# Kernel optimization log

Hardware: AMD Instinct MI355X
Metric: run time of the kernel (lower is better)

The kernel has to match this reference:

```python
import jax, jax.numpy as jnp
import numpy as np

N_SAMPLES = 64000
SAMPLE_RATE = 16000
DEPTH = 64              # bins per sinusoid in frequencies_softmax
HZ_MIN, HZ_MAX = 20.0, 8000.0


def exp_sigmoid(x, exponent=10.0, max_value=2.0, threshold=1e-7):
    # ddsp.core.exp_sigmoid
    return max_value * jax.nn.sigmoid(x) ** jnp.log(exponent) + threshold


def unit_to_hz(unit):
    # log-scale (midi) mapping of [0,1] -> [HZ_MIN, HZ_MAX]
    midi_min = 69.0 + 12.0 * np.log2(HZ_MIN / 440.0)
    midi_max = 69.0 + 12.0 * np.log2(HZ_MAX / 440.0)
    midi = midi_min + unit * (midi_max - midi_min)
    return 440.0 * 2.0 ** ((midi - 69.0) / 12.0)


def frequencies_softmax(logits):
    # ddsp.core.frequencies_softmax: softmax attention over DEPTH unit bins per sinusoid
    b, t, nd = logits.shape
    logits = logits.reshape(b, t, nd // DEPTH, DEPTH)
    probs = jax.nn.softmax(logits, axis=-1)
    bins = jnp.linspace(0.0, 1.0, DEPTH).astype(logits.dtype)
    f_unit = jnp.sum(probs * bins, axis=-1)          # [B, T, N]
    return unit_to_hz(f_unit)


def upsample_with_windows(x, n_timesteps):
    # ddsp.core.upsample_with_windows (add_endpoint=True): hann-window overlap-add at
    b, t, c = x.shape
    hop = n_timesteps // t
    xp = jnp.concatenate([x, x[:, -1:, :]], axis=1)  # pad endpoint frame -> [B, T+1, C]
    s = jnp.arange(n_timesteps)
    k = s // hop
    r = (s % hop).astype(x.dtype)
    w = 0.5 - 0.5 * jnp.cos(jnp.pi * r / hop)        # weight of next frame
    x0 = jnp.take(xp, k, axis=1)
    x1 = jnp.take(xp, k + 1, axis=1)
    return x0 * (1.0 - w)[None, :, None] + x1 * w[None, :, None]


def resample_linear(x, n_timesteps):
    # ddsp.core.resample(method='linear', add_endpoint=True): scale = T / n_timesteps
    b, t, c = x.shape
    src = jnp.arange(n_timesteps).astype(x.dtype) * (t / n_timesteps)
    i0 = jnp.clip(jnp.floor(src).astype(jnp.int32), 0, t - 1)
    i1 = jnp.clip(i0 + 1, 0, t - 1)
    frac = (src - i0.astype(x.dtype))[None, :, None]
    return jnp.take(x, i0, axis=1) * (1.0 - frac) + jnp.take(x, i1, axis=1) * frac


def setup_inputs() -> dict:
    key = jax.random.key(0)
    k1, k2 = jax.random.split(key)
    amplitudes = jax.random.normal(k1, (4, 250, 100), dtype=jnp.float32)
    frequencies = jax.random.normal(k2, (4, 250, 6400), dtype=jnp.float32)
    return {"amplitudes": amplitudes, "frequencies": frequencies}


def reference(amplitudes, frequencies):
    # get_controls
    amps = exp_sigmoid(amplitudes)                                   # [B, T, N]
    freqs = frequencies_softmax(frequencies)                         # [B, T, N] in Hz
    amps = amps * (freqs < SAMPLE_RATE / 2.0).astype(amps.dtype)     # remove_above_nyquist
    # get_signal
    amp_env = upsample_with_windows(amps, N_SAMPLES)                 # [B, S, N]
    freq_env = resample_linear(freqs, N_SAMPLES)                     # [B, S, N]
    omegas = freq_env * (2.0 * jnp.pi / SAMPLE_RATE)                 # rad/sample
    phases = jnp.cumsum(omegas, axis=1)                              # cumulative phase scan
    return jnp.sum(amp_env * jnp.sin(phases), axis=-1)               # [B, S]
```

## Files before the change

### kernel.cpp

```cpp
#include <hip/hip_runtime.h>
#include <math.h>


#define Bb 4
#define Tt 250
#define Nn 100
#define HOP 256
#define NSMP 64000

#define LOG2_400F 8.6438561897747247f

__global__ __launch_bounds__(256) void ctrl_kernel(
    const float* __restrict__ amp_in,
    const float* __restrict__ logits,
    float* __restrict__ fq,
    float* __restrict__ amp_out,
    int n_sids)
{
    const int wave = threadIdx.x >> 6;
    const int lane = threadIdx.x & 63;
    const int grp  = lane >> 4;
    const int sub  = lane & 15;
    const int sid  = blockIdx.x * 16 + wave * 4 + grp;
    if (sid >= n_sids) return;

    const float4 x4 = *(const float4*)(logits + (size_t)sid * 64 + sub * 4);

    const float e0 = __expf(x4.x);
    const float e1 = __expf(x4.y);
    const float e2 = __expf(x4.z);
    const float e3 = __expf(x4.w);
    const float bb = (float)(sub * 4);
    float den = (e0 + e1) + (e2 + e3);
    float num = e0 * bb + e1 * (bb + 1.0f) + e2 * (bb + 2.0f) + e3 * (bb + 3.0f);

#pragma unroll
    for (int off = 1; off < 16; off <<= 1) {
        num += __shfl_xor(num, off, 64);
        den += __shfl_xor(den, off, 64);
    }

    if (sub == 0) {
        const float u = num / (den * 63.0f);
        const float f = 20.0f * exp2f(u * LOG2_400F);
        fq[sid] = f;
        const float xa = amp_in[sid];
        const float sg = 1.0f / (1.0f + __expf(-xa));
        float av = 2.0f * __expf(2.3025851f * __logf(sg)) + 1e-7f;
        av = (f < 8000.0f) ? av : 0.0f;
        amp_out[sid] = av;
    }
}

__global__ __launch_bounds__(256) void scan_kernel(
    const float* __restrict__ fq,
    float* __restrict__ Pf)
{
    __shared__ double wtot[4];
    const int b = blockIdx.x / Nn;
    const int n = blockIdx.x % Nn;
    const int k = threadIdx.x;
    const int wave = k >> 6;
    const int lane = k & 63;

    double S = 0.0;
    if (k < Tt) {
        const int kp = (k + 1 < Tt) ? (k + 1) : (Tt - 1);
        const double f0 = (double)fq[(size_t)(b * Tt + k) * Nn + n];
        const double f1 = (double)fq[(size_t)(b * Tt + kp) * Nn + n];
        S = (256.0 * f0 + 127.5 * (f1 - f0)) * (1.0 / 16000.0);
    }

    double inc = S;
#pragma unroll
    for (int off = 1; off < 64; off <<= 1) {
        const double v = __shfl_up(inc, off, 64);
        if (lane >= off) inc += v;
    }
    if (lane == 63) wtot[wave] = inc;
    __syncthreads();

    double base = 0.0;
#pragma unroll
    for (int w = 0; w < 3; ++w)
        if (w < wave) base += wtot[w];

    if (k < Tt) {
        const double P = base + inc - S;
        Pf[(size_t)(b * Tt + k) * Nn + n] = (float)(P - floor(P));
    }
}

__global__ __launch_bounds__(256) void synth_kernel(
    const float* __restrict__ fq,
    const float* __restrict__ amp,
    const float* __restrict__ Pf,
    float* __restrict__ out)
{
    __shared__ float4 c4[2][Nn];
    __shared__ float  pfs[2][Nn];
    const int pair = blockIdx.x % (Tt / 2);
    const int b    = blockIdx.x / (Tt / 2);
    const int k0   = pair * 2;
    const int tid  = threadIdx.x;

    if (tid < 2 * Nn) {
        const int h = tid / Nn;
        const int n = tid % Nn;
        const int k = k0 + h;
        const int kp = (k + 1 < Tt) ? (k + 1) : (Tt - 1);
        const size_t i0 = (size_t)(b * Tt + k) * Nn + n;
        const size_t i1 = (size_t)(b * Tt + kp) * Nn + n;
        const float a0 = amp[i0];
        const float a1 = amp[i1];
        const float f0 = fq[i0];
        const float f1 = fq[i1];
        float4 c;
        c.x = a0;
        c.y = a1 - a0;
        c.z = f0 * (1.0f / 16000.0f);
        c.w = (f1 - f0) * (1.0f / (16000.0f * 256.0f));
        c4[h][n] = c;
        pfs[h][n] = Pf[i0];
    }
    __syncthreads();

    const int h  = tid >> 7;
    const int r0 = tid & 127;
    const int k  = k0 + h;
    const int rB = r0 + 128;

    const float wA = 0.5f - 0.5f * __builtin_amdgcn_cosf((float)r0 * (1.0f / 512.0f));
    const float wB = 0.5f - 0.5f * __builtin_amdgcn_cosf((float)rB * (1.0f / 512.0f));
    const float rp1A = (float)(r0 + 1);
    const float rp1B = (float)(rB + 1);
    const float triA = (float)(r0 * (r0 + 1) / 2);
    const float triB = (float)(rB * (rB + 1) / 2);

    float sumA = 0.0f, sumB = 0.0f;
#pragma unroll 4
    for (int n = 0; n < Nn; ++n) {
        const float4 c = c4[h][n];
        const float pf = pfs[h][n];
        const float aA = c.x + c.y * wA;
        const float aB = c.x + c.y * wB;
        float phA = pf + rp1A * c.z + triA * c.w;
        float phB = pf + rp1B * c.z + triB * c.w;
        phA -= floorf(phA);
        phB -= floorf(phB);
        sumA += aA * __builtin_amdgcn_sinf(phA);
        sumB += aB * __builtin_amdgcn_sinf(phB);
    }
    float* o = out + (size_t)b * NSMP + (size_t)k * HOP;
    o[r0] = sumA;
    o[rB] = sumB;
}

extern "C" void kernel_launch(void* const* d_in, const int* in_sizes, int n_in,
                              void* d_out, int out_size, void* d_ws, size_t ws_size,
                              hipStream_t stream) {
    const float* amps_in = (const float*)d_in[0];
    const float* logits  = (const float*)d_in[1];
    float* out = (float*)d_out;

    const int n_sids = in_sizes[0];
    char* ws = (char*)d_ws;
    float* fqw  = (float*)ws;
    float* ampw = (float*)(ws + 400000);
    float* Pf   = (float*)(ws + 800000);

    const int ctrl_blocks = (n_sids + 15) / 16;
    ctrl_kernel<<<dim3(ctrl_blocks), dim3(256), 0, stream>>>(amps_in, logits, fqw, ampw, n_sids);
    scan_kernel<<<dim3(Bb * Nn), dim3(256), 0, stream>>>(fqw, Pf);
    synth_kernel<<<dim3(Bb * (Tt / 2)), dim3(256), 0, stream>>>(fqw, ampw, Pf, out);
}
```

Baseline: 85.98 us.

## Fuse control and scan kernels and precompute packed synth coefficients

Merges the softmax/amplitude control kernel with the per-sinusoid phase scan so frequencies and amplitudes stay in shared memory instead of round-tripping through global memory. It also moves the construction of the packed float4 interpolation coefficients into the fused kernel, so the synth kernel just loads them. This removes a kernel launch and intermediate traffic. The cost is that each block now reads logits for one sinusoid across all frames with a strided pattern and lower parallelism (400 blocks), which may reduce memory throughput on the dominant logits read.

Measured after the change: 93.81 us. 1.09x slower.

```diff
diff --git a/kernel.cpp b/kernel.cpp
--- a/kernel.cpp
+++ b/kernel.cpp
@@ -10,67 +10,63 @@
 
 #define LOG2_400F 8.6438561897747247f
 
-__global__ __launch_bounds__(256) void ctrl_kernel(
+__global__ __launch_bounds__(256) void ctrl_scan_kernel(
     const float* __restrict__ amp_in,
     const float* __restrict__ logits,
-    float* __restrict__ fq,
-    float* __restrict__ amp_out,
-    int n_sids)
+    float4* __restrict__ c4pk,
+    float* __restrict__ pfk)
 {
-    const int wave = threadIdx.x >> 6;
-    const int lane = threadIdx.x & 63;
+    __shared__ float fs[256];
+    __shared__ float as[256];
+    __shared__ double wtot[4];
+    const int b    = blockIdx.x / Nn;
+    const int n    = blockIdx.x % Nn;
+    const int tid  = threadIdx.x;
+    const int wave = tid >> 6;
+    const int lane = tid & 63;
     const int grp  = lane >> 4;
     const int sub  = lane & 15;
-    const int sid  = blockIdx.x * 16 + wave * 4 + grp;
-    if (sid >= n_sids) return;
-
-    const float4 x4 = *(const float4*)(logits + (size_t)sid * 64 + sub * 4);
-
-    const float e0 = __expf(x4.x);
-    const float e1 = __expf(x4.y);
-    const float e2 = __expf(x4.z);
-    const float e3 = __expf(x4.w);
-    const float bb = (float)(sub * 4);
-    float den = (e0 + e1) + (e2 + e3);
-    float num = e0 * bb + e1 * (bb + 1.0f) + e2 * (bb + 2.0f) + e3 * (bb + 3.0f);
 
 #pragma unroll
-    for (int off = 1; off < 16; off <<= 1) {
-        num += __shfl_xor(num, off, 64);
-        den += __shfl_xor(den, off, 64);
+    for (int i = 0; i < 16; ++i) {
+        const int fk = i * 16 + wave * 4 + grp;
+        float4 x4 = make_float4(0.f, 0.f, 0.f, 0.f);
+        if (fk < Tt)
+            x4 = *(const float4*)(logits + ((size_t)(b * Tt + fk) * Nn + n) * 64 + sub * 4);
+
+        const float e0 = __expf(x4.x);
+        const float e1 = __expf(x4.y);
+        const float e2 = __expf(x4.z);
+        const float e3 = __expf(x4.w);
+        const float bb = (float)(sub * 4);
+        float den = (e0 + e1) + (e2 + e3);
+        float num = e0 * bb + e1 * (bb + 1.0f) + e2 * (bb + 2.0f) + e3 * (bb + 3.0f);
+#pragma unroll
+        for (int off = 1; off < 16; off <<= 1) {
+            num += __shfl_xor(num, off, 64);
+            den += __shfl_xor(den, off, 64);
+        }
+
+        if (sub == 0 && fk < Tt) {
+            const float u = num / (den * 63.0f);
+            const float f = 20.0f * exp2f(u * LOG2_400F);
+            fs[fk] = f;
+            const float xa = amp_in[(size_t)(b * Tt + fk) * Nn + n];
+            const float sg = 1.0f / (1.0f + __expf(-xa));
+            float av = 2.0f * __expf(2.3025851f * __logf(sg)) + 1e-7f;
+            as[fk] = (f < 8000.0f) ? av : 0.0f;
+        }
     }
+    __syncthreads();
 
-    if (sub == 0) {
-        const float u = num / (den * 63.0f);
-        const float f = 20.0f * exp2f(u * LOG2_400F);
-        fq[sid] = f;
-        const float xa = amp_in[sid];
-        const float sg = 1.0f / (1.0f + __expf(-xa));
-        float av = 2.0f * __expf(2.3025851f * __logf(sg)) + 1e-7f;
-        av = (f < 8000.0f) ? av : 0.0f;
-        amp_out[sid] = av;
-    }
-}
-
-__global__ __launch_bounds__(256) void scan_kernel(
-    const float* __restrict__ fq,
-    float* __restrict__ Pf)
-{
-    __shared__ double wtot[4];
-    const int b = blockIdx.x / Nn;
-    const int n = blockIdx.x % Nn;
-    const int k = threadIdx.x;
-    const int wave = k >> 6;
-    const int lane = k & 63;
-
+    const int k = tid;
     double S = 0.0;
     if (k < Tt) {
         const int kp = (k + 1 < Tt) ? (k + 1) : (Tt - 1);
-        const double f0 = (double)fq[(size_t)(b * Tt + k) * Nn + n];
-        const double f1 = (double)fq[(size_t)(b * Tt + kp) * Nn + n];
+        const double f0 = (double)fs[k];
+        const double f1 = (double)fs[kp];
         S = (256.0 * f0 + 127.5 * (f1 - f0)) * (1.0 / 16000.0);
     }
-
     double inc = S;
 #pragma unroll
     for (int off = 1; off < 64; off <<= 1) {
@@ -79,7 +75,6 @@
     }
     if (lane == 63) wtot[wave] = inc;
     __syncthreads();
-
     double base = 0.0;
 #pragma unroll
     for (int w = 0; w < 3; ++w)
@@ -87,14 +82,23 @@
 
     if (k < Tt) {
         const double P = base + inc - S;
-        Pf[(size_t)(b * Tt + k) * Nn + n] = (float)(P - floor(P));
+        const int kp = (k + 1 < Tt) ? (k + 1) : (Tt - 1);
+        const float a0 = as[k];
+        const float f0 = fs[k];
+        float4 c;
+        c.x = a0;
+        c.y = as[kp] - a0;
+        c.z = f0 * (1.0f / 16000.0f);
+        c.w = (fs[kp] - f0) * (1.0f / (16000.0f * 256.0f));
+        const size_t idx = (size_t)(b * Tt + k) * Nn + n;
+        c4pk[idx] = c;
+        pfk[idx] = (float)(P - floor(P));
     }
 }
 
 __global__ __launch_bounds__(256) void synth_kernel(
-    const float* __restrict__ fq,
-    const float* __restrict__ amp,
-    const float* __restrict__ Pf,
+    const float4* __restrict__ c4pk,
+    const float* __restrict__ pfk,
     float* __restrict__ out)
 {
     __shared__ float4 c4[2][Nn];
@@ -107,21 +111,9 @@
     if (tid < 2 * Nn) {
         const int h = tid / Nn;
         const int n = tid % Nn;
-        const int k = k0 + h;
-        const int kp = (k + 1 < Tt) ? (k + 1) : (Tt - 1);
-        const size_t i0 = (size_t)(b * Tt + k) * Nn + n;
-        const size_t i1 = (size_t)(b * Tt + kp) * Nn + n;
-        const float a0 = amp[i0];
-        const float a1 = amp[i1];
-        const float f0 = fq[i0];
-        const float f1 = fq[i1];
-        float4 c;
-        c.x = a0;
-        c.y = a1 - a0;
-        c.z = f0 * (1.0f / 16000.0f);
-        c.w = (f1 - f0) * (1.0f / (16000.0f * 256.0f));
-        c4[h][n] = c;
-        pfs[h][n] = Pf[i0];
+        const size_t idx = (size_t)(b * Tt + k0 + h) * Nn + n;
+        c4[h][n]  = c4pk[idx];
+        pfs[h][n] = pfk[idx];
     }
     __syncthreads();
 
@@ -163,14 +155,10 @@
     const float* logits  = (const float*)d_in[1];
     float* out = (float*)d_out;
 
-    const int n_sids = in_sizes[0];
     char* ws = (char*)d_ws;
-    float* fqw  = (float*)ws;
-    float* ampw = (float*)(ws + 400000);
-    float* Pf   = (float*)(ws + 800000);
+    float4* c4pk = (float4*)ws;
+    float*  pfk  = (float*)(ws + 1600000);
 
-    const int ctrl_blocks = (n_sids + 15) / 16;
-    ctrl_kernel<<<dim3(ctrl_blocks), dim3(256), 0, stream>>>(amps_in, logits, fqw, ampw, n_sids);
-    scan_kernel<<<dim3(Bb * Nn), dim3(256), 0, stream>>>(fqw, Pf);
-    synth_kernel<<<dim3(Bb * (Tt / 2)), dim3(256), 0, stream>>>(fqw, ampw, Pf, out);
+    ctrl_scan_kernel<<<dim3(Bb * Nn), dim3(256), 0, stream>>>(amps_in, logits, c4pk, pfk);
+    synth_kernel<<<dim3(Bb * (Tt / 2)), dim3(256), 0, stream>>>(c4pk, pfk, out);
 }
```
